# Kernel optimization log

Hardware: AMD Instinct MI355X
Metric: run time of the kernel (lower is better)

## Reference

```python
import jax, jax.numpy as jnp
import numpy as np

B, T, D, K = 8, 2048, 384, 64

def setup_inputs() -> dict:
    key = jax.random.key(0)
    k1, k2, k3, k4 = jax.random.split(key, 4)
    x = jax.random.normal(k1, (B, T, D), dtype=jnp.float32)
    # torch nn.Linear default init scale ~ 1/sqrt(fan_in); use scaled normals
    Wq = jax.random.normal(k2, (D, K), dtype=jnp.float32) / np.sqrt(D)
    Wk = jax.random.normal(k3, (D, K), dtype=jnp.float32) / np.sqrt(D)
    Wv = jax.random.normal(k4, (D, D), dtype=jnp.float32) / np.sqrt(D)
    return {"x": x, "Wq": Wq, "Wk": Wk, "Wv": Wv}

def reference(x, Wq, Wk, Wv):
    # x: (B,T,D)
    q = jnp.einsum('btd,dk->btk', x, Wq)      # (B,T,K)
    k = jnp.einsum('btd,dk->btk', x, Wk)      # (B,T,K)
    v = jnp.einsum('btd,de->bte', x, Wv)      # (B,T,D)
    scores = jnp.einsum('bqk,bsk->bqs', q, k) / jnp.sqrt(jnp.float32(K))  # (B,T,T)
    causal = jnp.tril(jnp.ones((T, T), dtype=bool))
    scores = jnp.where(causal, scores, -jnp.inf)
    weights = jax.nn.softmax(scores, axis=-1)
    out = jnp.einsum('bqs,bse->bqe', weights, v)  # (B,T,D)
    return out
```

## Files before the change

### kernel.cpp

```cpp
#include <hip/hip_runtime.h>

#define TT 2048
#define DD 384

typedef float f32x4 __attribute__((ext_vector_type(4)));
typedef float f32x16 __attribute__((ext_vector_type(16)));
typedef short s16x8 __attribute__((ext_vector_type(8)));
typedef short s16x2 __attribute__((ext_vector_type(2)));
typedef unsigned int u32x4 __attribute__((ext_vector_type(4)));
typedef unsigned int u32x2 __attribute__((ext_vector_type(2)));

typedef __attribute__((address_space(3))) unsigned char* as3p;
typedef const __attribute__((address_space(1))) unsigned char* as1p;
#define GLLDS(gsrc, ldst) __builtin_amdgcn_global_load_lds((as1p)(gsrc), (as3p)(ldst), 16, 0, 0)

static __device__ __forceinline__ unsigned short f2bf(float f) {
    unsigned int u = __builtin_bit_cast(unsigned int, f);
    u = (u + 0x7fffu + ((u >> 16) & 1u)) >> 16;
    return (unsigned short)u;
}
static __device__ __forceinline__ unsigned int pk2(float a, float b) {
#if __has_builtin(__builtin_amdgcn_cvt_pk_bf16_f32)
    s16x2 t = __builtin_amdgcn_cvt_pk_bf16_f32(a, b);
    return __builtin_bit_cast(unsigned int, t);
#else
    unsigned int ua = __builtin_bit_cast(unsigned int, a);
    unsigned int ub = __builtin_bit_cast(unsigned int, b);
    ua = (ua + 0x7fffu + ((ua >> 16) & 1u)) >> 16;
    ub = (ub + 0x7fffu + ((ub >> 16) & 1u)) & 0xffff0000u;
    return ua | ub;
#endif
}

__global__ __launch_bounds__(256, 8) void wprep(
    const float* __restrict__ Wq, const float* __restrict__ Wk, const float* __restrict__ Wv,
    unsigned short* __restrict__ wall)
{
    const int gid = blockIdx.x * 256 + threadIdx.x;
    const int col = gid & 511;
    const int kt  = gid >> 9;
    unsigned short* op = wall + (size_t)col * 384 + kt * 32;
    #pragma unroll
    for (int c = 0; c < 4; ++c) {
        u32x4 v;
        #pragma unroll
        for (int j2 = 0; j2 < 4; ++j2) {
            const int k = kt * 32 + c * 8 + j2 * 2;
            float f0 = (col < 64)  ? Wq[(size_t)k * 64 + col]
                     : (col < 128) ? Wk[(size_t)k * 64 + (col - 64)]
                                   : Wv[(size_t)k * 384 + (col - 128)];
            float f1 = (col < 64)  ? Wq[(size_t)(k + 1) * 64 + col]
                     : (col < 128) ? Wk[(size_t)(k + 1) * 64 + (col - 64)]
                                   : Wv[(size_t)(k + 1) * 384 + (col - 128)];
            v[j2] = pk2(f0, f1);
        }
        *(s16x8*)(op + ((c ^ (col & 3)) * 8)) = __builtin_bit_cast(s16x8, v);
    }
}

__global__ __launch_bounds__(256, 4) void qkv_gemm(
    const float* __restrict__ x, const unsigned short* __restrict__ wall,
    unsigned short* __restrict__ qo, unsigned short* __restrict__ ko,
    unsigned short* __restrict__ vto)
{
    __shared__ __align__(16) unsigned short lds[12288];
    const int tid = threadIdx.x;
    const int l   = tid & 63;
    const int w   = tid >> 6;
    const int si  = l & 15;
    const int qq  = l >> 4;
    const int m0  = blockIdx.x * 64;
    const int nb  = blockIdx.y;
    const int wr  = w >> 1, wc = w & 1;

    const int ar = tid >> 2, ac = tid & 3;
    const float* xs = x + (size_t)(m0 + ar) * DD + ac * 8;
    const unsigned short* ws = wall + (size_t)nb * 128 * 384;

#define QSTAGE(KT, B)                                                                      \
    {                                                                                      \
        _Pragma("unroll")                                                                  \
        for (int c2 = 0; c2 < 2; ++c2) {                                                   \
            const int ch = w * 2 + c2;                                                     \
            GLLDS(ws + (size_t)(ch * 16 + (l >> 2)) * 384 + (KT) * 32 + (l & 3) * 8,       \
                  &lds[(B) * 6144 + 2048 + ch * 512]);                                     \
        }                                                                                  \
        f32x4 x0 = *(const f32x4*)(xs + (KT) * 32);                                        \
        f32x4 x1 = *(const f32x4*)(xs + (KT) * 32 + 4);                                    \
        u32x4 av = (u32x4){pk2(x0[0], x0[1]), pk2(x0[2], x0[3]),                           \
                           pk2(x1[0], x1[1]), pk2(x1[2], x1[3])};                          \
        *(s16x8*)&lds[(B) * 6144 + ar * 32 + ((ac ^ (ar & 3)) * 8)] =                      \
            __builtin_bit_cast(s16x8, av);                                                 \
    }

    f32x4 acc[2][4];
    #pragma unroll
    for (int rt = 0; rt < 2; ++rt)
        #pragma unroll
        for (int ct = 0; ct < 4; ++ct) acc[rt][ct] = (f32x4){0.f, 0.f, 0.f, 0.f};

    QSTAGE(0, 0);
    for (int kt = 0; kt < 12; ++kt) {
        const int b = kt & 1;
        __syncthreads();
        if (kt < 11) QSTAGE(kt + 1, 1 - b);

        s16x8 af[2], bf[4];
        #pragma unroll
        for (int rt = 0; rt < 2; ++rt) {
            const int row = wr * 32 + rt * 16 + si;
            af[rt] = *(const s16x8*)&lds[b * 6144 + row * 32 + ((qq ^ (row & 3)) * 8)];
        }
        #pragma unroll
        for (int ct = 0; ct < 4; ++ct) {
            const int col = wc * 64 + ct * 16 + si;
            bf[ct] = *(const s16x8*)&lds[b * 6144 + 2048 + col * 32 + ((qq ^ (col & 3)) * 8)];
        }
        #pragma unroll
        for (int rt = 0; rt < 2; ++rt)
            #pragma unroll
            for (int ct = 0; ct < 4; ++ct)
                acc[rt][ct] = __builtin_amdgcn_mfma_f32_16x16x32_bf16(af[rt], bf[ct], acc[rt][ct], 0, 0, 0);
    }
    __syncthreads();
#undef QSTAGE

    if (nb == 0) {
        if (wc == 0) {
            #pragma unroll
            for (int rt = 0; rt < 2; ++rt)
                #pragma unroll
                for (int ct = 0; ct < 4; ++ct)
                    #pragma unroll
                    for (int r = 0; r < 4; ++r) {
                        const int m = m0 + wr * 32 + rt * 16 + qq * 4 + r;
                        qo[(size_t)m * 64 + ct * 16 + si] = f2bf(acc[rt][ct][r] * 0.125f);
                    }
        } else {
            #pragma unroll
            for (int rt = 0; rt < 2; ++rt)
                #pragma unroll
                for (int ct = 0; ct < 4; ++ct)
                    #pragma unroll
                    for (int r = 0; r < 4; ++r) {
                        const int m = m0 + wr * 32 + rt * 16 + qq * 4 + r;
                        const int col = ct * 16 + si;
                        ko[(size_t)m * 64 + (((col >> 3) ^ (m & 7)) * 8) + (col & 7)] = f2bf(acc[rt][ct][r]);
                    }
        }
    } else {
        #pragma unroll
        for (int rt = 0; rt < 2; ++rt)
            #pragma unroll
            for (int ct = 0; ct < 4; ++ct)
                #pragma unroll
                for (int r = 0; r < 4; ++r) {
                    const int m = wr * 32 + rt * 16 + qq * 4 + r;
                    const int n = wc * 64 + ct * 16 + si;
                    lds[n * 64 + (((m >> 3) ^ (n & 7)) * 8) + (m & 7)] = f2bf(acc[rt][ct][r]);
                }
        __syncthreads();
        const int bbat = m0 >> 11, t0 = m0 & 2047;
        #pragma unroll
        for (int i = 0; i < 4; ++i) {
            const int u = tid + 256 * i, n = u >> 3, p = u & 7;
            *(s16x8*)&vto[((size_t)bbat * DD + ((nb - 1) * 128 + n)) * TT + t0 + p * 8]
                = *(const s16x8*)&lds[n * 64 + p * 8];
        }
    }
}

__global__ __launch_bounds__(768, 3) void attn(
    const unsigned short* __restrict__ qg, const unsigned short* __restrict__ kg,
    const unsigned short* __restrict__ vg, float* __restrict__ out)
{
    __shared__ __align__(16) unsigned short lds[53248];

    const int tid = threadIdx.x;
    const int l   = tid & 63;
    const int w   = tid >> 6;
    const int qh  = w & 1;
    const int eu  = w >> 1;
    const bool isprod = (w < 4);
    const int lo  = l & 31;
    const int hi  = l >> 5;

    const int g  = blockIdx.x;
    const int bb = g & 7;
    const int eh = (g >> 3) & 1;
    const int pr = g >> 4;
    const int e0 = eh * 192;

    const unsigned short* kbase = kg + (size_t)bb * TT * 64;
    const unsigned short* vbase = vg + ((size_t)bb * DD + e0) * TT;

    #define STAGE(IT, KB, VB)                                                              \
    {                                                                                      \
        if (isprod) {                                                                      \
            GLLDS(kbase + (size_t)(IT) * 4096 + (2 * w) * 512 + l * 8,                     \
                  &lds[(KB) * 4096 + (2 * w) * 512]);                                      \
            GLLDS(kbase + (size_t)(IT) * 4096 + (2 * w + 1) * 512 + l * 8,                 \
                  &lds[(KB) * 4096 + (2 * w + 1) * 512]);                                  \
        } else {                                                                           \
            _Pragma("unroll")                                                              \
            for (int c3 = 0; c3 < 3; ++c3) {                                               \
                const int rg = 3 * (w - 4) + c3;                                           \
                GLLDS(vbase + (size_t)(rg * 8 + (l >> 3)) * TT + (IT) * 64 + (l & 7) * 8,  \
                      &lds[8192 + (VB) * 12288 + rg * 512]);                               \
            }                                                                              \
        }                                                                                  \
    }

    #define PVSTEP(VB, PB)                                                                 \
    {                                                                                      \
        __builtin_amdgcn_s_setprio(1);                                                     \
        _Pragma("unroll")                                                                  \
        for (int ss = 0; ss < 2; ++ss) {                                                   \
            const int pbse = 45056 + (PB) * 4096 + (qh * 2 + ss) * 1024;                   \
            s16x8 a0 = *(const s16x8*)&lds[pbse + l * 8];                                  \
            s16x8 a1 = *(const s16x8*)&lds[pbse + 512 + l * 8];                            \
            const int el = eu * 32 + lo;                                                   \
            const int vbse = 8192 + (VB) * 12288 + el * 64;                                \
            s16x8 v0 = *(const s16x8*)&lds[vbse + (((ss * 4 + hi) ^ (el & 7)) * 8)];       \
            o = __builtin_amdgcn_mfma_f32_32x32x16_bf16(a0, v0, o, 0, 0, 0);               \
            s16x8 v1 = *(const s16x8*)&lds[vbse + (((ss * 4 + 2 + hi) ^ (el & 7)) * 8)];   \
            o = __builtin_amdgcn_mfma_f32_32x32x16_bf16(a1, v1, o, 0, 0, 0);               \
        }                                                                                  \
        __builtin_amdgcn_s_setprio(0);                                                     \
    }

    for (int hf = 0; hf < 2; ++hf) {
        const int q2 = hf ? pr : 31 - pr;
        const int q0 = q2 * 64;
        const int qrow = q0 + qh * 32 + lo;

        s16x8 qf[4];
        if (isprod) {
            const unsigned short* qp = qg + ((size_t)bb * TT + qrow) * 64;
            #pragma unroll
            for (int st = 0; st < 4; ++st) qf[st] = *(const s16x8*)(qp + st * 16 + hi * 8);
        }

        f32x16 o;
        #pragma unroll
        for (int r = 0; r < 16; ++r) o[r] = 0.f;
        float lp = 0.f;

        STAGE(0, 0, 0);

        int vi = 0, vn = 1;
        for (int it = 0; it <= q2; ++it) {
            const int kb = it & 1;
            __syncthreads();

            if (it < q2) STAGE(it + 1, 1 - kb, vn);

            if (isprod) {
                f32x16 sa;
                #pragma unroll
                for (int r = 0; r < 16; ++r) sa[r] = 0.f;
                __builtin_amdgcn_s_setprio(1);
                #pragma unroll
                for (int st = 0; st < 4; ++st) {
                    s16x8 kf = *(const s16x8*)&lds[kb * 4096 + (eu * 32 + lo) * 64 + (((st * 2 + hi) ^ (lo & 7)) * 8)];
                    sa = __builtin_amdgcn_mfma_f32_32x32x16_bf16(kf, qf[st], sa, 0, 0, 0);
                }
                __builtin_amdgcn_s_setprio(0);
                const bool mb = (it == q2);
                float pv[16];
                #pragma unroll
                for (int r = 0; r < 16; ++r) {
                    float e = __expf(sa[r]);
                    if (mb) {
                        const int srow = it * 64 + eu * 32 + (r & 3) + 8 * (r >> 2) + 4 * hi;
                        if (srow > qrow) e = 0.f;
                    }
                    pv[r] = e;
                    lp += e;
                }
                unsigned int d0 = pk2(pv[0], pv[1]),   d1 = pk2(pv[2], pv[3]);
                unsigned int d2 = pk2(pv[4], pv[5]),   d3 = pk2(pv[6], pv[7]);
                unsigned int d4 = pk2(pv[8], pv[9]),   d5 = pk2(pv[10], pv[11]);
                unsigned int d6 = pk2(pv[12], pv[13]), d7 = pk2(pv[14], pv[15]);
                u32x4 fa0, fa1;
#if __has_builtin(__builtin_amdgcn_permlane32_swap)
                {
                    u32x2 s02 = __builtin_bit_cast(u32x2, __builtin_amdgcn_permlane32_swap(d0, d2, false, false));
                    u32x2 s13 = __builtin_bit_cast(u32x2, __builtin_amdgcn_permlane32_swap(d1, d3, false, false));
                    u32x2 s46 = __builtin_bit_cast(u32x2, __builtin_amdgcn_permlane32_swap(d4, d6, false, false));
                    u32x2 s57 = __builtin_bit_cast(u32x2, __builtin_amdgcn_permlane32_swap(d5, d7, false, false));
                    fa0 = (u32x4){s02[0], s13[0], s02[1], s13[1]};
                    fa1 = (u32x4){s46[0], s57[0], s46[1], s57[1]};
                }
#else
                {
                    unsigned int sA0 = hi ? d0 : d2, sA1 = hi ? d1 : d3;
                    unsigned int rA0 = (unsigned int)__shfl_xor((int)sA0, 32);
                    unsigned int rA1 = (unsigned int)__shfl_xor((int)sA1, 32);
                    fa0 = hi ? (u32x4){rA0, rA1, d2, d3} : (u32x4){d0, d1, rA0, rA1};
                    unsigned int sB0 = hi ? d4 : d6, sB1 = hi ? d5 : d7;
                    unsigned int rB0 = (unsigned int)__shfl_xor((int)sB0, 32);
                    unsigned int rB1 = (unsigned int)__shfl_xor((int)sB1, 32);
                    fa1 = hi ? (u32x4){rB0, rB1, d6, d7} : (u32x4){d4, d5, rB0, rB1};
                }
#endif
                *(s16x8*)&lds[45056 + kb * 4096 + (qh * 2 + eu) * 1024 + l * 8]       = __builtin_bit_cast(s16x8, fa0);
                *(s16x8*)&lds[45056 + kb * 4096 + (qh * 2 + eu) * 1024 + 512 + l * 8] = __builtin_bit_cast(s16x8, fa1);
            }

            if (it > 0) {
                const int vp = (vi == 0) ? 2 : vi - 1;
                PVSTEP(vp, 1 - kb);
            }

            vi = vn; vn = (vn == 2) ? 0 : vn + 1;
        }
        __syncthreads();
        {
            const int vlast = (vi == 0) ? 2 : vi - 1;
            PVSTEP(vlast, q2 & 1);
        }
        if (isprod) {
            float lt = lp + __shfl_xor(lp, 32);
            if (hi == 0) ((float*)lds)[(qh * 2 + eu) * 32 + lo] = lt;
        }
        __syncthreads();

        {
            const float* stL = (const float*)lds;
            #pragma unroll
            for (int r = 0; r < 16; ++r) {
                const int rloc = (r & 3) + 8 * (r >> 2) + 4 * hi;
                const float linv = 1.f / (stL[(qh * 2) * 32 + rloc] + stL[(qh * 2 + 1) * 32 + rloc]);
                out[((size_t)bb * TT + q0 + qh * 32 + rloc) * DD + e0 + eu * 32 + lo]
                    = o[r] * linv;
            }
        }
        __syncthreads();
    }
    #undef STAGE
    #undef PVSTEP
}

extern "C" void kernel_launch(void* const* d_in, const int* in_sizes, int n_in,
                              void* d_out, int out_size, void* d_ws, size_t ws_size,
                              hipStream_t stream)
{
    const float* x  = (const float*)d_in[0];
    const float* Wq = (const float*)d_in[1];
    const float* Wk = (const float*)d_in[2];
    const float* Wv = (const float*)d_in[3];

    unsigned short* qws  = (unsigned short*)d_ws;
    unsigned short* kws  = (unsigned short*)((char*)d_ws + ((size_t)2 << 20));
    unsigned short* vtws = (unsigned short*)((char*)d_ws + ((size_t)4 << 20));
    unsigned short* wall = (unsigned short*)((char*)d_ws + ((size_t)16 << 20));

    wprep<<<dim3(24), dim3(256), 0, stream>>>(Wq, Wk, Wv, wall);
    qkv_gemm<<<dim3(256, 4), dim3(256), 0, stream>>>(x, wall, qws, kws, vtws);
    attn<<<dim3(256), dim3(768), 0, stream>>>(qws, kws, vtws, (float*)d_out);
}
```

Before: 128.5 us.

## Pre-convert x to bf16 and split MFMA accumulators into independent chains

Adds an xprep kernel that converts x to swizzled bf16 once, so qkv_gemm can stage its A tiles with global_load_lds instead of reading fp32 and converting in registers for every N-block. It also splits the QK and PV MFMA accumulations in the attention kernel into two independent accumulators, shortening dependent MFMA chains at the cost of extra registers and an add. The trade-off is an extra launch plus a bf16 round trip of x through memory, and higher register pressure in attn.

New measurement: 135.3 us. 5.3% more time.

```diff
diff --git a/kernel.cpp b/kernel.cpp
--- a/kernel.cpp
+++ b/kernel.cpp
@@ -32,6 +32,20 @@
 #endif
 }
 
+__global__ __launch_bounds__(256, 8) void xprep(
+    const float* __restrict__ x, unsigned short* __restrict__ xbf)
+{
+    const int gid = blockIdx.x * 256 + threadIdx.x;
+    const int m  = gid / 48;
+    const int cc = gid % 48;
+    const int kt = cc >> 2, c = cc & 3;
+    const float* xp = x + (size_t)m * 384 + kt * 32 + c * 8;
+    f32x4 a = *(const f32x4*)xp;
+    f32x4 b = *(const f32x4*)(xp + 4);
+    u32x4 v = (u32x4){pk2(a[0], a[1]), pk2(a[2], a[3]), pk2(b[0], b[1]), pk2(b[2], b[3])};
+    *(s16x8*)(xbf + (size_t)m * 384 + kt * 32 + ((c ^ (m & 3)) * 8)) = __builtin_bit_cast(s16x8, v);
+}
+
 __global__ __launch_bounds__(256, 8) void wprep(
     const float* __restrict__ Wq, const float* __restrict__ Wk, const float* __restrict__ Wv,
     unsigned short* __restrict__ wall)
@@ -59,7 +73,7 @@
 }
 
 __global__ __launch_bounds__(256, 4) void qkv_gemm(
-    const float* __restrict__ x, const unsigned short* __restrict__ wall,
+    const unsigned short* __restrict__ xbf, const unsigned short* __restrict__ wall,
     unsigned short* __restrict__ qo, unsigned short* __restrict__ ko,
     unsigned short* __restrict__ vto)
 {
@@ -73,24 +87,19 @@
     const int nb  = blockIdx.y;
     const int wr  = w >> 1, wc = w & 1;
 
-    const int ar = tid >> 2, ac = tid & 3;
-    const float* xs = x + (size_t)(m0 + ar) * DD + ac * 8;
+    const unsigned short* as = xbf + (size_t)m0 * 384;
     const unsigned short* ws = wall + (size_t)nb * 128 * 384;
 
 #define QSTAGE(KT, B)                                                                      \
     {                                                                                      \
+        GLLDS(as + (size_t)(w * 16 + (l >> 2)) * 384 + (KT) * 32 + (l & 3) * 8,            \
+              &lds[(B) * 6144 + w * 512]);                                                 \
         _Pragma("unroll")                                                                  \
         for (int c2 = 0; c2 < 2; ++c2) {                                                   \
             const int ch = w * 2 + c2;                                                     \
             GLLDS(ws + (size_t)(ch * 16 + (l >> 2)) * 384 + (KT) * 32 + (l & 3) * 8,       \
                   &lds[(B) * 6144 + 2048 + ch * 512]);                                     \
         }                                                                                  \
-        f32x4 x0 = *(const f32x4*)(xs + (KT) * 32);                                        \
-        f32x4 x1 = *(const f32x4*)(xs + (KT) * 32 + 4);                                    \
-        u32x4 av = (u32x4){pk2(x0[0], x0[1]), pk2(x0[2], x0[3]),                           \
-                           pk2(x1[0], x1[1]), pk2(x1[2], x1[3])};                          \
-        *(s16x8*)&lds[(B) * 6144 + ar * 32 + ((ac ^ (ar & 3)) * 8)] =                      \
-            __builtin_bit_cast(s16x8, av);                                                 \
     }
 
     f32x4 acc[2][4];
@@ -214,17 +223,25 @@
     #define PVSTEP(VB, PB)                                                                 \
     {                                                                                      \
         __builtin_amdgcn_s_setprio(1);                                                     \
-        _Pragma("unroll")                                                                  \
-        for (int ss = 0; ss < 2; ++ss) {                                                   \
-            const int pbse = 45056 + (PB) * 4096 + (qh * 2 + ss) * 1024;                   \
+        const int el = eu * 32 + lo;                                                       \
+        const int vbse = 8192 + (VB) * 12288 + el * 64;                                    \
+        {                                                                                  \
+            const int pbse = 45056 + (PB) * 4096 + (qh * 2 + 0) * 1024;                    \
             s16x8 a0 = *(const s16x8*)&lds[pbse + l * 8];                                  \
             s16x8 a1 = *(const s16x8*)&lds[pbse + 512 + l * 8];                            \
-            const int el = eu * 32 + lo;                                                   \
-            const int vbse = 8192 + (VB) * 12288 + el * 64;                                \
-            s16x8 v0 = *(const s16x8*)&lds[vbse + (((ss * 4 + hi) ^ (el & 7)) * 8)];       \
-            o = __builtin_amdgcn_mfma_f32_32x32x16_bf16(a0, v0, o, 0, 0, 0);               \
-            s16x8 v1 = *(const s16x8*)&lds[vbse + (((ss * 4 + 2 + hi) ^ (el & 7)) * 8)];   \
-            o = __builtin_amdgcn_mfma_f32_32x32x16_bf16(a1, v1, o, 0, 0, 0);               \
+            s16x8 v0 = *(const s16x8*)&lds[vbse + (((0 + hi) ^ (el & 7)) * 8)];            \
+            oa = __builtin_amdgcn_mfma_f32_32x32x16_bf16(a0, v0, oa, 0, 0, 0);             \
+            s16x8 v1 = *(const s16x8*)&lds[vbse + (((2 + hi) ^ (el & 7)) * 8)];            \
+            oa = __builtin_amdgcn_mfma_f32_32x32x16_bf16(a1, v1, oa, 0, 0, 0);             \
+        }                                                                                  \
+        {                                                                                  \
+            const int pbse = 45056 + (PB) * 4096 + (qh * 2 + 1) * 1024;                    \
+            s16x8 a0 = *(const s16x8*)&lds[pbse + l * 8];                                  \
+            s16x8 a1 = *(const s16x8*)&lds[pbse + 512 + l * 8];                            \
+            s16x8 v0 = *(const s16x8*)&lds[vbse + (((4 + hi) ^ (el & 7)) * 8)];            \
+            ob = __builtin_amdgcn_mfma_f32_32x32x16_bf16(a0, v0, ob, 0, 0, 0);             \
+            s16x8 v1 = *(const s16x8*)&lds[vbse + (((6 + hi) ^ (el & 7)) * 8)];            \
+            ob = __builtin_amdgcn_mfma_f32_32x32x16_bf16(a1, v1, ob, 0, 0, 0);             \
         }                                                                                  \
         __builtin_amdgcn_s_setprio(0);                                                     \
     }
@@ -241,9 +258,9 @@
             for (int st = 0; st < 4; ++st) qf[st] = *(const s16x8*)(qp + st * 16 + hi * 8);
         }
 
-        f32x16 o;
-        #pragma unroll
-        for (int r = 0; r < 16; ++r) o[r] = 0.f;
+        f32x16 oa, ob;
+        #pragma unroll
+        for (int r = 0; r < 16; ++r) { oa[r] = 0.f; ob[r] = 0.f; }
         float lp = 0.f;
 
         STAGE(0, 0, 0);
@@ -256,21 +273,26 @@
             if (it < q2) STAGE(it + 1, 1 - kb, vn);
 
             if (isprod) {
-                f32x16 sa;
-                #pragma unroll
-                for (int r = 0; r < 16; ++r) sa[r] = 0.f;
+                f32x16 sa0, sa1;
+                #pragma unroll
+                for (int r = 0; r < 16; ++r) { sa0[r] = 0.f; sa1[r] = 0.f; }
                 __builtin_amdgcn_s_setprio(1);
-                #pragma unroll
-                for (int st = 0; st < 4; ++st) {
-                    s16x8 kf = *(const s16x8*)&lds[kb * 4096 + (eu * 32 + lo) * 64 + (((st * 2 + hi) ^ (lo & 7)) * 8)];
-                    sa = __builtin_amdgcn_mfma_f32_32x32x16_bf16(kf, qf[st], sa, 0, 0, 0);
+                {
+                    s16x8 kf0 = *(const s16x8*)&lds[kb * 4096 + (eu * 32 + lo) * 64 + (((0 + hi) ^ (lo & 7)) * 8)];
+                    sa0 = __builtin_amdgcn_mfma_f32_32x32x16_bf16(kf0, qf[0], sa0, 0, 0, 0);
+                    s16x8 kf1 = *(const s16x8*)&lds[kb * 4096 + (eu * 32 + lo) * 64 + (((2 + hi) ^ (lo & 7)) * 8)];
+                    sa0 = __builtin_amdgcn_mfma_f32_32x32x16_bf16(kf1, qf[1], sa0, 0, 0, 0);
+                    s16x8 kf2 = *(const s16x8*)&lds[kb * 4096 + (eu * 32 + lo) * 64 + (((4 + hi) ^ (lo & 7)) * 8)];
+                    sa1 = __builtin_amdgcn_mfma_f32_32x32x16_bf16(kf2, qf[2], sa1, 0, 0, 0);
+                    s16x8 kf3 = *(const s16x8*)&lds[kb * 4096 + (eu * 32 + lo) * 64 + (((6 + hi) ^ (lo & 7)) * 8)];
+                    sa1 = __builtin_amdgcn_mfma_f32_32x32x16_bf16(kf3, qf[3], sa1, 0, 0, 0);
                 }
                 __builtin_amdgcn_s_setprio(0);
                 const bool mb = (it == q2);
                 float pv[16];
                 #pragma unroll
                 for (int r = 0; r < 16; ++r) {
-                    float e = __expf(sa[r]);
+                    float e = __expf(sa0[r] + sa1[r]);
                     if (mb) {
                         const int srow = it * 64 + eu * 32 + (r & 3) + 8 * (r >> 2) + 4 * hi;
                         if (srow > qrow) e = 0.f;
@@ -333,7 +355,7 @@
                 const int rloc = (r & 3) + 8 * (r >> 2) + 4 * hi;
                 const float linv = 1.f / (stL[(qh * 2) * 32 + rloc] + stL[(qh * 2 + 1) * 32 + rloc]);
                 out[((size_t)bb * TT + q0 + qh * 32 + rloc) * DD + e0 + eu * 32 + lo]
-                    = o[r] * linv;
+                    = (oa[r] + ob[r]) * linv;
             }
         }
         __syncthreads();
@@ -354,9 +376,11 @@
     unsigned short* qws  = (unsigned short*)d_ws;
     unsigned short* kws  = (unsigned short*)((char*)d_ws + ((size_t)2 << 20));
     unsigned short* vtws = (unsigned short*)((char*)d_ws + ((size_t)4 << 20));
-    unsigned short* wall = (unsigned short*)((char*)d_ws + ((size_t)16 << 20));
-
+    unsigned short* xbf  = (unsigned short*)((char*)d_ws + ((size_t)16 << 20));
+    unsigned short* wall = (unsigned short*)((char*)d_ws + ((size_t)28 << 20));
+
+    xprep<<<dim3(3072), dim3(256), 0, stream>>>(x, xbf);
     wprep<<<dim3(24), dim3(256), 0, stream>>>(Wq, Wk, Wv, wall);
-    qkv_gemm<<<dim3(256, 4), dim3(256), 0, stream>>>(x, wall, qws, kws, vtws);
+    qkv_gemm<<<dim3(256, 4), dim3(256), 0, stream>>>(xbf, wall, qws, kws, vtws);
     attn<<<dim3(256), dim3(768), 0, stream>>>(qws, kws, vtws, (float*)d_out);
 }
```

## Split attention waves into QK/softmax producers and dedicated PV consumer waves

Applied to the files above, without the earlier changes.

Raises the attention block from 12 to 16 waves. The first four waves now only compute QK^T, exp and the P tiles. Twelve dedicated waves stage V and run the PV MFMAs and the output normalisation, where before all waves shared the PV and output work. The aim is to overlap softmax work with PV matrix work across specialised waves instead of serialising them inside the producer waves. The launch bound now asks for 4 blocks of 1024 threads per CU, which tightens the register budget and could cause spills, even though LDS use already limits residency to one block per CU.

Result: faster. 126.0 us (-2.0%).

```diff
diff --git a/kernel.cpp b/kernel.cpp
--- a/kernel.cpp
+++ b/kernel.cpp
@@ -170,7 +170,7 @@
     }
 }
 
-__global__ __launch_bounds__(768, 3) void attn(
+__global__ __launch_bounds__(1024, 4) void attn(
     const unsigned short* __restrict__ qg, const unsigned short* __restrict__ kg,
     const unsigned short* __restrict__ vg, float* __restrict__ out)
 {
@@ -179,9 +179,9 @@
     const int tid = threadIdx.x;
     const int l   = tid & 63;
     const int w   = tid >> 6;
-    const int qh  = w & 1;
-    const int eu  = w >> 1;
     const bool isprod = (w < 4);
+    const int qh  = isprod ? (w & 1) : ((w - 4) & 1);
+    const int su  = isprod ? (w >> 1) : ((w - 4) >> 1);
     const int lo  = l & 31;
     const int hi  = l >> 5;
 
@@ -203,8 +203,8 @@
                   &lds[(KB) * 4096 + (2 * w + 1) * 512]);                                  \
         } else {                                                                           \
             _Pragma("unroll")                                                              \
-            for (int c3 = 0; c3 < 3; ++c3) {                                               \
-                const int rg = 3 * (w - 4) + c3;                                           \
+            for (int c2 = 0; c2 < 2; ++c2) {                                               \
+                const int rg = 2 * (w - 4) + c2;                                           \
                 GLLDS(vbase + (size_t)(rg * 8 + (l >> 3)) * TT + (IT) * 64 + (l & 7) * 8,  \
                       &lds[8192 + (VB) * 12288 + rg * 512]);                               \
             }                                                                              \
@@ -219,7 +219,7 @@
             const int pbse = 45056 + (PB) * 4096 + (qh * 2 + ss) * 1024;                   \
             s16x8 a0 = *(const s16x8*)&lds[pbse + l * 8];                                  \
             s16x8 a1 = *(const s16x8*)&lds[pbse + 512 + l * 8];                            \
-            const int el = eu * 32 + lo;                                                   \
+            const int el = su * 32 + lo;                                                   \
             const int vbse = 8192 + (VB) * 12288 + el * 64;                                \
             s16x8 v0 = *(const s16x8*)&lds[vbse + (((ss * 4 + hi) ^ (el & 7)) * 8)];       \
             o = __builtin_amdgcn_mfma_f32_32x32x16_bf16(a0, v0, o, 0, 0, 0);               \
@@ -262,7 +262,7 @@
                 __builtin_amdgcn_s_setprio(1);
                 #pragma unroll
                 for (int st = 0; st < 4; ++st) {
-                    s16x8 kf = *(const s16x8*)&lds[kb * 4096 + (eu * 32 + lo) * 64 + (((st * 2 + hi) ^ (lo & 7)) * 8)];
+                    s16x8 kf = *(const s16x8*)&lds[kb * 4096 + (su * 32 + lo) * 64 + (((st * 2 + hi) ^ (lo & 7)) * 8)];
                     sa = __builtin_amdgcn_mfma_f32_32x32x16_bf16(kf, qf[st], sa, 0, 0, 0);
                 }
                 __builtin_amdgcn_s_setprio(0);
@@ -272,7 +272,7 @@
                 for (int r = 0; r < 16; ++r) {
                     float e = __expf(sa[r]);
                     if (mb) {
-                        const int srow = it * 64 + eu * 32 + (r & 3) + 8 * (r >> 2) + 4 * hi;
+                        const int srow = it * 64 + su * 32 + (r & 3) + 8 * (r >> 2) + 4 * hi;
                         if (srow > qrow) e = 0.f;
                     }
                     pv[r] = e;
@@ -304,11 +304,9 @@
                     fa1 = hi ? (u32x4){rB0, rB1, d6, d7} : (u32x4){d4, d5, rB0, rB1};
                 }
 #endif
-                *(s16x8*)&lds[45056 + kb * 4096 + (qh * 2 + eu) * 1024 + l * 8]       = __builtin_bit_cast(s16x8, fa0);
-                *(s16x8*)&lds[45056 + kb * 4096 + (qh * 2 + eu) * 1024 + 512 + l * 8] = __builtin_bit_cast(s16x8, fa1);
-            }
-
-            if (it > 0) {
+                *(s16x8*)&lds[45056 + kb * 4096 + (qh * 2 + su) * 1024 + l * 8]       = __builtin_bit_cast(s16x8, fa0);
+                *(s16x8*)&lds[45056 + kb * 4096 + (qh * 2 + su) * 1024 + 512 + l * 8] = __builtin_bit_cast(s16x8, fa1);
+            } else if (it > 0) {
                 const int vp = (vi == 0) ? 2 : vi - 1;
                 PVSTEP(vp, 1 - kb);
             }
@@ -316,23 +314,23 @@
             vi = vn; vn = (vn == 2) ? 0 : vn + 1;
         }
         __syncthreads();
-        {
+
+        if (isprod) {
+            float lt = lp + __shfl_xor(lp, 32);
+            if (hi == 0) ((float*)lds)[(qh * 2 + su) * 32 + lo] = lt;
+        } else {
             const int vlast = (vi == 0) ? 2 : vi - 1;
             PVSTEP(vlast, q2 & 1);
         }
-        if (isprod) {
-            float lt = lp + __shfl_xor(lp, 32);
-            if (hi == 0) ((float*)lds)[(qh * 2 + eu) * 32 + lo] = lt;
-        }
-        __syncthreads();
-
-        {
+        __syncthreads();
+
+        if (!isprod) {
             const float* stL = (const float*)lds;
             #pragma unroll
             for (int r = 0; r < 16; ++r) {
                 const int rloc = (r & 3) + 8 * (r >> 2) + 4 * hi;
                 const float linv = 1.f / (stL[(qh * 2) * 32 + rloc] + stL[(qh * 2 + 1) * 32 + rloc]);
-                out[((size_t)bb * TT + q0 + qh * 32 + rloc) * DD + e0 + eu * 32 + lo]
+                out[((size_t)bb * TT + q0 + qh * 32 + rloc) * DD + e0 + su * 32 + lo]
                     = o[r] * linv;
             }
         }
@@ -358,5 +356,5 @@
 
     wprep<<<dim3(24), dim3(256), 0, stream>>>(Wq, Wk, Wv, wall);
     qkv_gemm<<<dim3(256, 4), dim3(256), 0, stream>>>(x, wall, qws, kws, vtws);
-    attn<<<dim3(256), dim3(768), 0, stream>>>(qws, kws, vtws, (float*)d_out);
-}
+    attn<<<dim3(256), dim3(1024), 0, stream>>>(qws, kws, vtws, (float*)d_out);
+}
```
